# Performance work log

Measured on AMD Instinct MI355X. Metric: run time of the kernel, lower is better.

## Reference

```python
import jax, jax.numpy as jnp
import numpy as np

N = 16        # state dim n
M = 8         # control dim m
T = 50        # time_steps
DT = 0.01     # delta_t
SQRT_DT = DT ** 0.5
GAMMA = 0.1
SIGMA = 0.2
TAU = 0.5
H = 10        # hidden width of subnets
BATCH = 32768


def _mlp(params, x):
    W1, b1, W2, b2, W3, b3 = params
    h = jnp.tanh(x @ W1 + b1)
    h = jnp.tanh(h @ W2 + b2)
    return h @ W3 + b3


def setup_inputs() -> dict:
    key = jax.random.key(0)
    ks = jax.random.split(key, 32)

    def dense(k, i, o):
        return (jax.random.normal(k, (i, o), jnp.float32) / np.float32(np.sqrt(i)))

    inp = {
        'dw': jax.random.normal(ks[0], (T, BATCH, 1), jnp.float32) * SQRT_DT,
        'X0': jax.random.uniform(ks[1], (BATCH, N), jnp.float32),
        'A': dense(ks[2], N, N),
        'Bmat': dense(ks[3], N, M),
        'Cmat': dense(ks[4], N, N),
        'Dmat': dense(ks[5], N, M),
        # phi: (n+1) -> 10 -> 10 -> m
        'phi_W1': dense(ks[6], N + 1, H), 'phi_b1': jnp.zeros((H,), jnp.float32),
        'phi_W2': dense(ks[7], H, H),     'phi_b2': jnp.zeros((H,), jnp.float32),
        'phi_W3': dense(ks[8], H, M),     'phi_b3': jnp.zeros((M,), jnp.float32),
        # Z: (n+1) -> 10 -> 10 -> n
        'Z_W1': dense(ks[9], N + 1, H),   'Z_b1': jnp.zeros((H,), jnp.float32),
        'Z_W2': dense(ks[10], H, H),      'Z_b2': jnp.zeros((H,), jnp.float32),
        'Z_W3': dense(ks[11], H, N),      'Z_b3': jnp.zeros((N,), jnp.float32),
        # Y0: n -> 10 -> 10 -> n
        'Y0_W1': dense(ks[12], N, H),     'Y0_b1': jnp.zeros((H,), jnp.float32),
        'Y0_W2': dense(ks[13], H, H),     'Y0_b2': jnp.zeros((H,), jnp.float32),
        'Y0_W3': dense(ks[14], H, N),     'Y0_b3': jnp.zeros((N,), jnp.float32),
    }
    return inp


def reference(dw, X0, A, Bmat, Cmat, Dmat,
              phi_W1, phi_b1, phi_W2, phi_b2, phi_W3, phi_b3,
              Z_W1, Z_b1, Z_W2, Z_b2, Z_W3, Z_b3,
              Y0_W1, Y0_b1, Y0_W2, Y0_b2, Y0_W3, Y0_b3):
    phi_p = (phi_W1, phi_b1, phi_W2, phi_b2, phi_W3, phi_b3)
    Z_p = (Z_W1, Z_b1, Z_W2, Z_b2, Z_W3, Z_b3)
    Y0_p = (Y0_W1, Y0_b1, Y0_W2, Y0_b2, Y0_W3, Y0_b3)

    B = X0.shape[0]
    Y = _mlp(Y0_p, X0)                              # [B, n]
    t_grid = jnp.arange(T, dtype=X0.dtype) * DT     # [T]
    w_trap = jnp.ones((T,), X0.dtype).at[1:-1].set(2.0)  # trapezoid weights

    def step(carry, xs):
        X, Yc, lc = carry
        dwi, t, w = xs                              # dwi: [B,1]
        state = jnp.concatenate(
            [jnp.broadcast_to(t, (B, 1)).astype(X.dtype), X], axis=1)  # [B, n+1]
        Zv = _mlp(Z_p, state)                       # [B, n]
        u = _mlp(phi_p, state)                      # [B, m] (project = identity)
        # b_mult(M, x) == x @ M.T
        drift_X = X @ A.T + u @ Bmat.T + GAMMA      # [B, n]
        diffusion_X = X @ Cmat.T + u @ Dmat.T + SIGMA
        drift_Y = -(Yc @ A + Zv @ Cmat + X)         # f_x(X,u) = X
        # stop_recording branch: gradient of dH / pre_phi
        dH = Yc @ Bmat + Zv @ Dmat + u              # f_u(X,u) = u -> [B, m]
        pre_phi = jax.lax.stop_gradient(u - TAU * dH)
        Xn = X + drift_X * DT + dwi * diffusion_X
        Yn = Yc + drift_Y * DT + dwi * Zv
        lc = lc + 0.5 * DT * w * jnp.sum(jnp.square(u - pre_phi), axis=1)
        return (Xn, Yn, lc), None

    init = (X0, Y, jnp.zeros((B,), X0.dtype))
    (X, Y, loss_control), _ = jax.lax.scan(step, init, (dw, t_grid, w_trap))
    loss_bsde = jnp.sum(jnp.square(Y - X), axis=1)  # g_x(X) = X
    return jnp.stack([jnp.mean(loss_bsde), jnp.mean(loss_control)])
```

## Files before the change

kernel.cpp:

```cpp
#include <hip/hip_runtime.h>

namespace {

typedef float v4f __attribute__((ext_vector_type(4)));
typedef _Float16 half8 __attribute__((ext_vector_type(8)));
typedef unsigned int uint32;

constexpr int   kB     = 32768;
constexpr int   kT     = 50;
constexpr float kDT    = 0.01f;
constexpr float kGamma = 0.1f;
constexpr float kSigma = 0.2f;
constexpr float kTau   = 0.5f;
constexpr float kA     = 2.8853900817779268f;

constexpr int kWsDwords = 13 * 256;

__device__ __forceinline__ float fact(float x) {
  return __builtin_amdgcn_rcpf(exp2f(x) + 1.0f);
}

__device__ __forceinline__ uint32 pk2(float a, float b) {
  union { _Float16 h[2]; uint32 u; } z;
  z.h[0] = (_Float16)a; z.h[1] = (_Float16)b;
  return z.u;
}

__device__ __forceinline__ v4f act4(v4f a) {
  v4f r;
  r[0] = fact(a[0]); r[1] = fact(a[1]);
  r[2] = fact(a[2]); r[3] = fact(a[3]);
  return r;
}

union U8 { uint32 u[4]; half8 h; };

__global__ __launch_bounds__(256) void prep_kernel(
    const float* __restrict__ A,   const float* __restrict__ Bm,
    const float* __restrict__ Cm,  const float* __restrict__ Dm,
    const float* __restrict__ pW1, const float* __restrict__ pb1,
    const float* __restrict__ pW2, const float* __restrict__ pb2,
    const float* __restrict__ pW3, const float* __restrict__ pb3,
    const float* __restrict__ zW1, const float* __restrict__ zb1,
    const float* __restrict__ zW2, const float* __restrict__ zb2,
    const float* __restrict__ zW3, const float* __restrict__ zb3,
    const float* __restrict__ yW1, const float* __restrict__ yb1,
    const float* __restrict__ yW2, const float* __restrict__ yb2,
    const float* __restrict__ yW3, const float* __restrict__ yb3,
    uint32* __restrict__ ws, float* __restrict__ out)
{
  const int tid = threadIdx.x;
  if (tid < 2) out[tid] = 0.0f;

  auto sum10 = [](const float* W, int stride, int m) {
    float s = 0.f;
    for (int j = 0; j < 10; ++j) s += W[j * stride + m];
    return s;
  };

  auto wval = [&](int p, int m, int k) -> float {
    switch (p) {
      case 0:
        if (m >= 10) return 0.f;
        if (k < 16) return kA * yW1[k * 10 + m];
        if (k == 17) return kA * yb1[m];
        return 0.f;
      case 1:
        if (m >= 10) return 0.f;
        if (k < 10) return -2.f * kA * yW2[k * 10 + m];
        if (k == 10) return kA * (yb2[m] + sum10(yW2, 10, m));
        return 0.f;
      case 2:
        if (k < 10) return -2.f * yW3[k * 16 + m];
        if (k == 10) return yb3[m] + sum10(yW3, 16, m);
        return 0.f;
      case 3:
        if (m >= 10) return 0.f;
        if (k < 16) return kA * zW1[(k + 1) * 10 + m];
        if (k == 16) return kA * zW1[m];
        if (k == 17) return kA * zb1[m];
        return 0.f;
      case 4:
        if (m >= 10) return 0.f;
        if (k < 16) return kA * pW1[(k + 1) * 10 + m];
        if (k == 16) return kA * pW1[m];
        if (k == 17) return kA * pb1[m];
        return 0.f;
      case 5:
        if (m >= 10) return 0.f;
        if (k < 10) return -2.f * kA * zW2[k * 10 + m];
        if (k == 10) return kA * (zb2[m] + sum10(zW2, 10, m));
        return 0.f;
      case 6:
        if (m >= 10) return 0.f;
        if (k < 10) return -2.f * kA * pW2[k * 10 + m];
        if (k == 10) return kA * (pb2[m] + sum10(pW2, 10, m));
        return 0.f;
      case 7:
        if (k < 10) return -2.f * zW3[k * 16 + m];
        if (k == 10) return zb3[m] + sum10(zW3, 16, m);
        return 0.f;
      case 8:
        if (m >= 8) return 0.f;
        if (k < 10) return -2.f * pW3[k * 8 + m];
        if (k == 10) return pb3[m] + sum10(pW3, 8, m);
        return 0.f;
      case 9:
        if (k < 16) return A[m * 16 + k];
        if (k < 24) return Bm[m * 8 + (k - 16)];
        if (k == 24) return kGamma;
        return 0.f;
      case 10:
        if (k < 16) return Cm[m * 16 + k];
        if (k < 24) return Dm[m * 8 + (k - 16)];
        if (k == 24) return kSigma;
        return 0.f;
      case 11:
        if (k < 16) return A[k * 16 + m];
        return Cm[(k - 16) * 16 + m];
      case 12:
        if (m >= 8) return 0.f;
        if (k < 16) return Bm[k * 8 + m];
        return Dm[(k - 16) * 8 + m];
    }
    return 0.f;
  };

  for (int idx = tid; idx < kWsDwords; idx += 256) {
    int p = idx >> 8, r = idx & 255;
    int lane = r >> 2, dwi = r & 3;
    int m = lane & 15, q = lane >> 4;
    int k0 = 8 * q + 2 * dwi;
    ws[idx] = pk2(wval(p, m, k0), wval(p, m, k0 + 1));
  }
}

__global__ __launch_bounds__(64)
__attribute__((amdgpu_waves_per_eu(2, 2)))
void bsde_kernel(const float* __restrict__ dw, const float* __restrict__ X0,
                 const uint32* __restrict__ wsu, float* __restrict__ out)
{
  const int lane = threadIdx.x;
  const int col  = lane & 15;
  const int quad = lane >> 4;
  const int e    = blockIdx.x * 16 + col;

  half8 af[13];
#pragma unroll
  for (int p = 0; p < 13; ++p) {
    union { uint4 u; half8 h; } z;
    z.u = *(const uint4*)(wsu + p * 256 + lane * 4);
    af[p] = z.h;
  }

  const int srcA  = col + ((quad & 1) << 5);
  const int addrH = col + ((quad == 0) ? 16 : 32);
  const uint32 pkONE = pk2(1.f, 0.f);
  const v4f zero4 = {0.f, 0.f, 0.f, 0.f};

  auto shf = [](uint32 v, int s) -> uint32 {
    return (uint32)__shfl((int)v, s, 64);
  };

  auto buildH = [&](v4f th) -> half8 {
    uint32 lp0 = pk2(th[0], th[1]);
    uint32 lp1 = pk2(th[2], th[3]);
    uint32 bpA = shf(lp0, addrH);
    uint32 bpB = shf(lp1, addrH);
    U8 f;
    f.u[0] = (quad == 0) ? lp0 : ((quad == 1) ? bpA : 0u);
    f.u[1] = (quad == 0) ? lp1 : ((quad == 1) ? pkONE : 0u);
    f.u[2] = (quad == 0) ? bpA : 0u;
    f.u[3] = (quad == 0) ? bpB : 0u;
    return f.h;
  };

  v4f x4 = *(const v4f*)&X0[e * 16 + 4 * quad];
  v4f y4;
  {
    uint32 xp0 = pk2(x4[0], x4[1]), xp1 = pk2(x4[2], x4[3]);
    uint32 XD0 = shf(xp0, srcA),      XD1 = shf(xp1, srcA);
    uint32 XD2 = shf(xp0, srcA + 16), XD3 = shf(xp1, srcA + 16);
    uint32 pkT = pk2(0.f, 1.f);
    U8 b1;
    b1.u[0] = (quad < 2) ? XD0 : ((quad == 2) ? pkT : 0u);
    b1.u[1] = (quad < 2) ? XD1 : 0u;
    b1.u[2] = (quad < 2) ? XD2 : 0u;
    b1.u[3] = (quad < 2) ? XD3 : 0u;
    v4f h = __builtin_amdgcn_mfma_f32_16x16x32_f16(af[0], b1.h, zero4, 0, 0, 0);
    half8 hf = buildH(act4(h));
    v4f g = __builtin_amdgcn_mfma_f32_16x16x32_f16(af[1], hf, zero4, 0, 0, 0);
    half8 gf = buildH(act4(g));
    y4 = __builtin_amdgcn_mfma_f32_16x16x32_f16(af[2], gf, zero4, 0, 0, 0);
  }

  float lcp = 0.0f;
  float dwv = dw[e];

#pragma unroll 1
  for (int t = 0; t < kT; ++t) {
    float dwn = (t < kT - 1) ? dw[(t + 1) * kB + e] : 0.0f;
    const float tv = (float)t * kDT;
    const float wt = (t == 0 || t == kT - 1) ? 1.0f : 2.0f;

    uint32 xp0 = pk2(x4[0], x4[1]), xp1 = pk2(x4[2], x4[3]);
    uint32 yp0 = pk2(y4[0], y4[1]), yp1 = pk2(y4[2], y4[3]);
    uint32 XD0 = shf(xp0, srcA),      XD1 = shf(xp1, srcA);
    uint32 XD2 = shf(xp0, srcA + 16), XD3 = shf(xp1, srcA + 16);
    uint32 YD0 = shf(yp0, srcA),      YD1 = shf(yp1, srcA);
    uint32 YD2 = shf(yp0, srcA + 16), YD3 = shf(yp1, srcA + 16);

    uint32 pkT = pk2(tv, 1.f);
    U8 b1;
    b1.u[0] = (quad < 2) ? XD0 : ((quad == 2) ? pkT : 0u);
    b1.u[1] = (quad < 2) ? XD1 : 0u;
    b1.u[2] = (quad < 2) ? XD2 : 0u;
    b1.u[3] = (quad < 2) ? XD3 : 0u;

    v4f hz = __builtin_amdgcn_mfma_f32_16x16x32_f16(af[3], b1.h, zero4, 0, 0, 0);
    v4f hp = __builtin_amdgcn_mfma_f32_16x16x32_f16(af[4], b1.h, zero4, 0, 0, 0);
    half8 hzf = buildH(act4(hz));
    half8 hpf = buildH(act4(hp));

    v4f gz = __builtin_amdgcn_mfma_f32_16x16x32_f16(af[5], hzf, zero4, 0, 0, 0);
    v4f gp = __builtin_amdgcn_mfma_f32_16x16x32_f16(af[6], hpf, zero4, 0, 0, 0);
    half8 gzf = buildH(act4(gz));
    half8 gpf = buildH(act4(gp));

    v4f zv = __builtin_amdgcn_mfma_f32_16x16x32_f16(af[7], gzf, zero4, 0, 0, 0);
    v4f uu = __builtin_amdgcn_mfma_f32_16x16x32_f16(af[8], gpf, zero4, 0, 0, 0);

    uint32 up0 = pk2(uu[0], uu[1]), up1 = pk2(uu[2], uu[3]);
    uint32 zp0 = pk2(zv[0], zv[1]), zp1 = pk2(zv[2], zv[3]);
    uint32 UD0 = shf(up0, col),      UD1 = shf(up1, col);
    uint32 UD2 = shf(up0, col + 16), UD3 = shf(up1, col + 16);
    uint32 ZD0 = shf(zp0, srcA),      ZD1 = shf(zp1, srcA);
    uint32 ZD2 = shf(zp0, srcA + 16), ZD3 = shf(zp1, srcA + 16);

    U8 xu, yz;
    xu.u[0] = (quad < 2) ? XD0 : ((quad == 2) ? UD0 : pkONE);
    xu.u[1] = (quad < 2) ? XD1 : ((quad == 2) ? UD1 : 0u);
    xu.u[2] = (quad < 2) ? XD2 : ((quad == 2) ? UD2 : 0u);
    xu.u[3] = (quad < 2) ? XD3 : ((quad == 2) ? UD3 : 0u);
    yz.u[0] = (quad < 2) ? YD0 : ZD0;
    yz.u[1] = (quad < 2) ? YD1 : ZD1;
    yz.u[2] = (quad < 2) ? YD2 : ZD2;
    yz.u[3] = (quad < 2) ? YD3 : ZD3;

    v4f dx = __builtin_amdgcn_mfma_f32_16x16x32_f16(af[9],  xu.h, zero4, 0, 0, 0);
    v4f fx = __builtin_amdgcn_mfma_f32_16x16x32_f16(af[10], xu.h, zero4, 0, 0, 0);
    v4f dy = __builtin_amdgcn_mfma_f32_16x16x32_f16(af[11], yz.h, zero4, 0, 0, 0);
    v4f dh = __builtin_amdgcn_mfma_f32_16x16x32_f16(af[12], yz.h, zero4, 0, 0, 0);

    float ss = 0.0f;
    v4f Xn, Yn;
#pragma unroll
    for (int r = 0; r < 4; ++r) {
      Xn[r] = x4[r] + kDT * dx[r] + dwv * fx[r];
      Yn[r] = y4[r] - kDT * (dy[r] + x4[r]) + dwv * zv[r];
      float d = dh[r] + uu[r];
      ss += d * d;
    }
    lcp += (0.5f * kDT * kTau * kTau) * wt * ss;
    x4 = Xn; y4 = Yn;
    dwv = dwn;
  }

  float bp = 0.0f;
#pragma unroll
  for (int r = 0; r < 4; ++r) { float d = y4[r] - x4[r]; bp += d * d; }

#pragma unroll
  for (int s = 32; s > 0; s >>= 1) {
    bp  += __shfl_down(bp,  s, 64);
    lcp += __shfl_down(lcp, s, 64);
  }
  if (lane == 0) {
    atomicAdd(&out[0], bp  * (1.0f / (float)kB));
    atomicAdd(&out[1], lcp * (1.0f / (float)kB));
  }
}

}

extern "C" void kernel_launch(void* const* d_in, const int* in_sizes, int n_in,
                              void* d_out, int out_size, void* d_ws, size_t ws_size,
                              hipStream_t stream) {
  (void)in_sizes; (void)n_in; (void)ws_size; (void)out_size;

  const float* dw  = (const float*)d_in[0];
  const float* X0  = (const float*)d_in[1];
  const float* A   = (const float*)d_in[2];
  const float* Bm  = (const float*)d_in[3];
  const float* Cm  = (const float*)d_in[4];
  const float* Dm  = (const float*)d_in[5];
  const float* pW1 = (const float*)d_in[6];
  const float* pb1 = (const float*)d_in[7];
  const float* pW2 = (const float*)d_in[8];
  const float* pb2 = (const float*)d_in[9];
  const float* pW3 = (const float*)d_in[10];
  const float* pb3 = (const float*)d_in[11];
  const float* zW1 = (const float*)d_in[12];
  const float* zb1 = (const float*)d_in[13];
  const float* zW2 = (const float*)d_in[14];
  const float* zb2 = (const float*)d_in[15];
  const float* zW3 = (const float*)d_in[16];
  const float* zb3 = (const float*)d_in[17];
  const float* yW1 = (const float*)d_in[18];
  const float* yb1 = (const float*)d_in[19];
  const float* yW2 = (const float*)d_in[20];
  const float* yb2 = (const float*)d_in[21];
  const float* yW3 = (const float*)d_in[22];
  const float* yb3 = (const float*)d_in[23];
  float* out = (float*)d_out;
  unsigned int* ws = (unsigned int*)d_ws;

  prep_kernel<<<1, 256, 0, stream>>>(
      A, Bm, Cm, Dm,
      pW1, pb1, pW2, pb2, pW3, pb3,
      zW1, zb1, zW2, zb2, zW3, zb3,
      yW1, yb1, yW2, yb2, yW3, yb3, ws, out);

  bsde_kernel<<<kB / 16, 64, 0, stream>>>(dw, X0, ws, out);
}
```

Baseline: 211.1 us.

## Switch to 16x16x16 MFMA with C/D layout reuse, eliminating cross-lane shuffles

Replaces the 16x16x32 MFMAs with 16x16x16 MFMAs whose B-operand layout matches the accumulator output layout. Activations can then feed the next matmul directly without cross-lane shuffles or fragment assembly. Biases and time terms move into the accumulator input instead of constant-one rows in K. The concatenated matmuls are split into chained accumulations. This removes many ds_bpermute/shuffle ops and selects per step, at the cost of more, smaller MFMAs (17 weight fragments) on a serial dependency chain.

```diff
diff --git a/kernel.cpp b/kernel.cpp
--- a/kernel.cpp
+++ b/kernel.cpp
@@ -3,7 +3,7 @@
 namespace {
 
 typedef float v4f __attribute__((ext_vector_type(4)));
-typedef _Float16 half8 __attribute__((ext_vector_type(8)));
+typedef _Float16 half4 __attribute__((ext_vector_type(4)));
 typedef unsigned int uint32;
 
 constexpr int   kB     = 32768;
@@ -14,7 +14,9 @@
 constexpr float kTau   = 0.5f;
 constexpr float kA     = 2.8853900817779268f;
 
-constexpr int kWsDwords = 13 * 256;
+constexpr int kNFrag      = 17;
+constexpr int kFragDwords = kNFrag * 128;
+constexpr int kBiasFloats = 11 * 16;
 
 __device__ __forceinline__ float fact(float x) {
   return __builtin_amdgcn_rcpf(exp2f(x) + 1.0f);
@@ -32,8 +34,6 @@
   r[2] = fact(a[2]); r[3] = fact(a[3]);
   return r;
 }
-
-union U8 { uint32 u[4]; half8 h; };
 
 __global__ __launch_bounds__(256) void prep_kernel(
     const float* __restrict__ A,   const float* __restrict__ Bm,
@@ -60,78 +60,54 @@
 
   auto wval = [&](int p, int m, int k) -> float {
     switch (p) {
-      case 0:
-        if (m >= 10) return 0.f;
-        if (k < 16) return kA * yW1[k * 10 + m];
-        if (k == 17) return kA * yb1[m];
-        return 0.f;
-      case 1:
-        if (m >= 10) return 0.f;
-        if (k < 10) return -2.f * kA * yW2[k * 10 + m];
-        if (k == 10) return kA * (yb2[m] + sum10(yW2, 10, m));
-        return 0.f;
-      case 2:
-        if (k < 10) return -2.f * yW3[k * 16 + m];
-        if (k == 10) return yb3[m] + sum10(yW3, 16, m);
-        return 0.f;
-      case 3:
-        if (m >= 10) return 0.f;
-        if (k < 16) return kA * zW1[(k + 1) * 10 + m];
-        if (k == 16) return kA * zW1[m];
-        if (k == 17) return kA * zb1[m];
-        return 0.f;
-      case 4:
-        if (m >= 10) return 0.f;
-        if (k < 16) return kA * pW1[(k + 1) * 10 + m];
-        if (k == 16) return kA * pW1[m];
-        if (k == 17) return kA * pb1[m];
-        return 0.f;
-      case 5:
-        if (m >= 10) return 0.f;
-        if (k < 10) return -2.f * kA * zW2[k * 10 + m];
-        if (k == 10) return kA * (zb2[m] + sum10(zW2, 10, m));
-        return 0.f;
-      case 6:
-        if (m >= 10) return 0.f;
-        if (k < 10) return -2.f * kA * pW2[k * 10 + m];
-        if (k == 10) return kA * (pb2[m] + sum10(pW2, 10, m));
-        return 0.f;
-      case 7:
-        if (k < 10) return -2.f * zW3[k * 16 + m];
-        if (k == 10) return zb3[m] + sum10(zW3, 16, m);
-        return 0.f;
-      case 8:
-        if (m >= 8) return 0.f;
-        if (k < 10) return -2.f * pW3[k * 8 + m];
-        if (k == 10) return pb3[m] + sum10(pW3, 8, m);
-        return 0.f;
-      case 9:
-        if (k < 16) return A[m * 16 + k];
-        if (k < 24) return Bm[m * 8 + (k - 16)];
-        if (k == 24) return kGamma;
-        return 0.f;
-      case 10:
-        if (k < 16) return Cm[m * 16 + k];
-        if (k < 24) return Dm[m * 8 + (k - 16)];
-        if (k == 24) return kSigma;
-        return 0.f;
-      case 11:
-        if (k < 16) return A[k * 16 + m];
-        return Cm[(k - 16) * 16 + m];
-      case 12:
-        if (m >= 8) return 0.f;
-        if (k < 16) return Bm[k * 8 + m];
-        return Dm[(k - 16) * 8 + m];
+      case 0:  return (m < 10) ? kA * yW1[k * 10 + m] : 0.f;
+      case 1:  return (m < 10 && k < 10) ? -2.f * kA * yW2[k * 10 + m] : 0.f;
+      case 2:  return (k < 10) ? -2.f * yW3[k * 16 + m] : 0.f;
+      case 3:  return (m < 10) ? kA * zW1[(k + 1) * 10 + m] : 0.f;
+      case 4:  return (m < 10) ? kA * pW1[(k + 1) * 10 + m] : 0.f;
+      case 5:  return (m < 10 && k < 10) ? -2.f * kA * zW2[k * 10 + m] : 0.f;
+      case 6:  return (m < 10 && k < 10) ? -2.f * kA * pW2[k * 10 + m] : 0.f;
+      case 7:  return (k < 10) ? -2.f * zW3[k * 16 + m] : 0.f;
+      case 8:  return (m < 8 && k < 10) ? -2.f * pW3[k * 8 + m] : 0.f;
+      case 9:  return A[m * 16 + k];
+      case 10: return (k < 8) ? Bm[m * 8 + k] : 0.f;
+      case 11: return Cm[m * 16 + k];
+      case 12: return (k < 8) ? Dm[m * 8 + k] : 0.f;
+      case 13: return A[k * 16 + m];
+      case 14: return Cm[k * 16 + m];
+      case 15: return (m < 8) ? Bm[k * 8 + m] : 0.f;
+      case 16: return (m < 8) ? Dm[k * 8 + m] : 0.f;
     }
     return 0.f;
   };
 
-  for (int idx = tid; idx < kWsDwords; idx += 256) {
-    int p = idx >> 8, r = idx & 255;
-    int lane = r >> 2, dwi = r & 3;
+  for (int idx = tid; idx < kFragDwords; idx += 256) {
+    int p = idx >> 7, r = idx & 127;
+    int lane = r >> 1, dwi = r & 1;
     int m = lane & 15, q = lane >> 4;
-    int k0 = 8 * q + 2 * dwi;
+    int k0 = 4 * q + 2 * dwi;
     ws[idx] = pk2(wval(p, m, k0), wval(p, m, k0 + 1));
+  }
+
+  float* bsf = (float*)(ws + kFragDwords);
+  auto bval = [&](int a, int m) -> float {
+    switch (a) {
+      case 0:  return (m < 10) ? kA * yb1[m] : 0.f;
+      case 1:  return (m < 10) ? kA * (yb2[m] + sum10(yW2, 10, m)) : 0.f;
+      case 2:  return yb3[m] + sum10(yW3, 16, m);
+      case 3:  return (m < 10) ? kA * (zb2[m] + sum10(zW2, 10, m)) : 0.f;
+      case 4:  return (m < 10) ? kA * (pb2[m] + sum10(pW2, 10, m)) : 0.f;
+      case 5:  return zb3[m] + sum10(zW3, 16, m);
+      case 6:  return (m < 8) ? pb3[m] + sum10(pW3, 8, m) : 0.f;
+      case 7:  return (m < 10) ? kA * zW1[m] : 0.f;
+      case 8:  return (m < 10) ? kA * zb1[m] : 0.f;
+      case 9:  return (m < 10) ? kA * pW1[m] : 0.f;
+      case 10: return (m < 10) ? kA * pb1[m] : 0.f;
+    }
+    return 0.f;
+  };
+  for (int j = tid; j < kBiasFloats; j += 256) {
+    bsf[j] = bval(j >> 4, j & 15);
   }
 }
 
@@ -144,54 +120,50 @@
   const int col  = lane & 15;
   const int quad = lane >> 4;
   const int e    = blockIdx.x * 16 + col;
-
-  half8 af[13];
-#pragma unroll
-  for (int p = 0; p < 13; ++p) {
-    union { uint4 u; half8 h; } z;
-    z.u = *(const uint4*)(wsu + p * 256 + lane * 4);
+  const int bq   = quad * 4;
+
+  half4 af[kNFrag];
+#pragma unroll
+  for (int p = 0; p < kNFrag; ++p) {
+    union { uint2 u; half4 h; } z;
+    z.u = *(const uint2*)(wsu + p * 128 + lane * 2);
     af[p] = z.h;
   }
 
-  const int srcA  = col + ((quad & 1) << 5);
-  const int addrH = col + ((quad == 0) ? 16 : 32);
-  const uint32 pkONE = pk2(1.f, 0.f);
+  const float* bsf = (const float*)(wsu + kFragDwords);
+  const v4f c2z = *(const v4f*)&bsf[3 * 16 + bq];
+  const v4f c2p = *(const v4f*)&bsf[4 * 16 + bq];
+  const v4f c3z = *(const v4f*)&bsf[5 * 16 + bq];
+  const v4f c3p = *(const v4f*)&bsf[6 * 16 + bq];
+  const v4f vtz = *(const v4f*)&bsf[7 * 16 + bq];
+  const v4f vbz = *(const v4f*)&bsf[8 * 16 + bq];
+  const v4f vtp = *(const v4f*)&bsf[9 * 16 + bq];
+  const v4f vbp = *(const v4f*)&bsf[10 * 16 + bq];
+
+  auto pk4 = [](v4f a) -> half4 {
+    half4 h;
+    h[0] = (_Float16)a[0]; h[1] = (_Float16)a[1];
+    h[2] = (_Float16)a[2]; h[3] = (_Float16)a[3];
+    return h;
+  };
+  auto mm = [](half4 a, half4 b, v4f c) -> v4f {
+    return __builtin_amdgcn_mfma_f32_16x16x16f16(a, b, c, 0, 0, 0);
+  };
+
   const v4f zero4 = {0.f, 0.f, 0.f, 0.f};
-
-  auto shf = [](uint32 v, int s) -> uint32 {
-    return (uint32)__shfl((int)v, s, 64);
-  };
-
-  auto buildH = [&](v4f th) -> half8 {
-    uint32 lp0 = pk2(th[0], th[1]);
-    uint32 lp1 = pk2(th[2], th[3]);
-    uint32 bpA = shf(lp0, addrH);
-    uint32 bpB = shf(lp1, addrH);
-    U8 f;
-    f.u[0] = (quad == 0) ? lp0 : ((quad == 1) ? bpA : 0u);
-    f.u[1] = (quad == 0) ? lp1 : ((quad == 1) ? pkONE : 0u);
-    f.u[2] = (quad == 0) ? bpA : 0u;
-    f.u[3] = (quad == 0) ? bpB : 0u;
-    return f.h;
-  };
-
-  v4f x4 = *(const v4f*)&X0[e * 16 + 4 * quad];
+  const v4f gam4  = {kGamma, kGamma, kGamma, kGamma};
+  const v4f sig4  = {kSigma, kSigma, kSigma, kSigma};
+
+  v4f x4 = *(const v4f*)&X0[e * 16 + bq];
+  half4 xB = pk4(x4);
   v4f y4;
   {
-    uint32 xp0 = pk2(x4[0], x4[1]), xp1 = pk2(x4[2], x4[3]);
-    uint32 XD0 = shf(xp0, srcA),      XD1 = shf(xp1, srcA);
-    uint32 XD2 = shf(xp0, srcA + 16), XD3 = shf(xp1, srcA + 16);
-    uint32 pkT = pk2(0.f, 1.f);
-    U8 b1;
-    b1.u[0] = (quad < 2) ? XD0 : ((quad == 2) ? pkT : 0u);
-    b1.u[1] = (quad < 2) ? XD1 : 0u;
-    b1.u[2] = (quad < 2) ? XD2 : 0u;
-    b1.u[3] = (quad < 2) ? XD3 : 0u;
-    v4f h = __builtin_amdgcn_mfma_f32_16x16x32_f16(af[0], b1.h, zero4, 0, 0, 0);
-    half8 hf = buildH(act4(h));
-    v4f g = __builtin_amdgcn_mfma_f32_16x16x32_f16(af[1], hf, zero4, 0, 0, 0);
-    half8 gf = buildH(act4(g));
-    y4 = __builtin_amdgcn_mfma_f32_16x16x32_f16(af[2], gf, zero4, 0, 0, 0);
+    v4f cy1 = *(const v4f*)&bsf[0 * 16 + bq];
+    v4f cy2 = *(const v4f*)&bsf[1 * 16 + bq];
+    v4f cy3 = *(const v4f*)&bsf[2 * 16 + bq];
+    v4f h = mm(af[0], xB, cy1);
+    v4f g = mm(af[1], pk4(act4(h)), cy2);
+    y4    = mm(af[2], pk4(act4(g)), cy3);
   }
 
   float lcp = 0.0f;
@@ -203,54 +175,33 @@
     const float tv = (float)t * kDT;
     const float wt = (t == 0 || t == kT - 1) ? 1.0f : 2.0f;
 
-    uint32 xp0 = pk2(x4[0], x4[1]), xp1 = pk2(x4[2], x4[3]);
-    uint32 yp0 = pk2(y4[0], y4[1]), yp1 = pk2(y4[2], y4[3]);
-    uint32 XD0 = shf(xp0, srcA),      XD1 = shf(xp1, srcA);
-    uint32 XD2 = shf(xp0, srcA + 16), XD3 = shf(xp1, srcA + 16);
-    uint32 YD0 = shf(yp0, srcA),      YD1 = shf(yp1, srcA);
-    uint32 YD2 = shf(yp0, srcA + 16), YD3 = shf(yp1, srcA + 16);
-
-    uint32 pkT = pk2(tv, 1.f);
-    U8 b1;
-    b1.u[0] = (quad < 2) ? XD0 : ((quad == 2) ? pkT : 0u);
-    b1.u[1] = (quad < 2) ? XD1 : 0u;
-    b1.u[2] = (quad < 2) ? XD2 : 0u;
-    b1.u[3] = (quad < 2) ? XD3 : 0u;
-
-    v4f hz = __builtin_amdgcn_mfma_f32_16x16x32_f16(af[3], b1.h, zero4, 0, 0, 0);
-    v4f hp = __builtin_amdgcn_mfma_f32_16x16x32_f16(af[4], b1.h, zero4, 0, 0, 0);
-    half8 hzf = buildH(act4(hz));
-    half8 hpf = buildH(act4(hp));
-
-    v4f gz = __builtin_amdgcn_mfma_f32_16x16x32_f16(af[5], hzf, zero4, 0, 0, 0);
-    v4f gp = __builtin_amdgcn_mfma_f32_16x16x32_f16(af[6], hpf, zero4, 0, 0, 0);
-    half8 gzf = buildH(act4(gz));
-    half8 gpf = buildH(act4(gp));
-
-    v4f zv = __builtin_amdgcn_mfma_f32_16x16x32_f16(af[7], gzf, zero4, 0, 0, 0);
-    v4f uu = __builtin_amdgcn_mfma_f32_16x16x32_f16(af[8], gpf, zero4, 0, 0, 0);
-
-    uint32 up0 = pk2(uu[0], uu[1]), up1 = pk2(uu[2], uu[3]);
-    uint32 zp0 = pk2(zv[0], zv[1]), zp1 = pk2(zv[2], zv[3]);
-    uint32 UD0 = shf(up0, col),      UD1 = shf(up1, col);
-    uint32 UD2 = shf(up0, col + 16), UD3 = shf(up1, col + 16);
-    uint32 ZD0 = shf(zp0, srcA),      ZD1 = shf(zp1, srcA);
-    uint32 ZD2 = shf(zp0, srcA + 16), ZD3 = shf(zp1, srcA + 16);
-
-    U8 xu, yz;
-    xu.u[0] = (quad < 2) ? XD0 : ((quad == 2) ? UD0 : pkONE);
-    xu.u[1] = (quad < 2) ? XD1 : ((quad == 2) ? UD1 : 0u);
-    xu.u[2] = (quad < 2) ? XD2 : ((quad == 2) ? UD2 : 0u);
-    xu.u[3] = (quad < 2) ? XD3 : ((quad == 2) ? UD3 : 0u);
-    yz.u[0] = (quad < 2) ? YD0 : ZD0;
-    yz.u[1] = (quad < 2) ? YD1 : ZD1;
-    yz.u[2] = (quad < 2) ? YD2 : ZD2;
-    yz.u[3] = (quad < 2) ? YD3 : ZD3;
-
-    v4f dx = __builtin_amdgcn_mfma_f32_16x16x32_f16(af[9],  xu.h, zero4, 0, 0, 0);
-    v4f fx = __builtin_amdgcn_mfma_f32_16x16x32_f16(af[10], xu.h, zero4, 0, 0, 0);
-    v4f dy = __builtin_amdgcn_mfma_f32_16x16x32_f16(af[11], yz.h, zero4, 0, 0, 0);
-    v4f dh = __builtin_amdgcn_mfma_f32_16x16x32_f16(af[12], yz.h, zero4, 0, 0, 0);
+    half4 yB = pk4(y4);
+
+    v4f dx1 = mm(af[9],  xB, gam4);
+    v4f fx1 = mm(af[11], xB, sig4);
+    v4f dy1 = mm(af[13], yB, zero4);
+    v4f dh1 = mm(af[15], yB, zero4);
+
+    v4f c1z, c1p;
+#pragma unroll
+    for (int r = 0; r < 4; ++r) {
+      c1z[r] = vbz[r] + tv * vtz[r];
+      c1p[r] = vbp[r] + tv * vtp[r];
+    }
+
+    v4f hz = mm(af[3], xB, c1z);
+    v4f hp = mm(af[4], xB, c1p);
+    v4f gz = mm(af[5], pk4(act4(hz)), c2z);
+    v4f gp = mm(af[6], pk4(act4(hp)), c2p);
+    v4f zv = mm(af[7], pk4(act4(gz)), c3z);
+    v4f uu = mm(af[8], pk4(act4(gp)), c3p);
+
+    half4 zB = pk4(zv);
+    half4 uB = pk4(uu);
+    v4f dx = mm(af[10], uB, dx1);
+    v4f fx = mm(af[12], uB, fx1);
+    v4f dy = mm(af[14], zB, dy1);
+    v4f dh = mm(af[16], zB, dh1);
 
     float ss = 0.0f;
     v4f Xn, Yn;
@@ -263,6 +214,7 @@
     }
     lcp += (0.5f * kDT * kTau * kTau) * wt * ss;
     x4 = Xn; y4 = Yn;
+    xB = pk4(x4);
     dwv = dwn;
   }
 
```

After: 191.2 us. 1.1x faster.
